# Optimization experiments

Measured on AMD Instinct MI355X. Metric: run time of the kernel, lower is better.

Reference implementation:

```python
import jax, jax.numpy as jnp
import numpy as np

N = 100_000          # nodes
E = 1_600_000        # edges
ORIG = 92            # orig_atom_fea_len
NBR = 41             # nbr_fea_len (RBF bins)
ATOM = 64            # atom_fea_len
NCONV = 3
H = 128              # h_fea_len
OUT = 1
NGRAPH = 256         # graphs in batch
ZDIM = 2 * ATOM + NBR  # CGConv concat dim = 169
RBF_VMIN, RBF_VMAX = 0.0, 8.0


def setup_inputs() -> dict:
    key = jax.random.key(0)
    ks = jax.random.split(key, 12)
    s = lambda fan: float(1.0 / np.sqrt(fan))
    u = lambda k, shape, fan: jax.random.uniform(k, shape, jnp.float32, -s(fan), s(fan))
    return {
        "x": jax.random.normal(ks[0], (N, ORIG), jnp.float32),
        "edge_attr": jax.random.normal(ks[1], (E, 3), jnp.float32),
        "W_emb": u(ks[2], (ORIG, ATOM), ORIG),
        "b_emb": u(ks[3], (ATOM,), ORIG),
        "Wf": u(ks[4], (NCONV, ZDIM, ATOM), ZDIM),
        "bf": u(ks[5], (NCONV, ATOM), ZDIM),
        "Ws": u(ks[6], (NCONV, ZDIM, ATOM), ZDIM),
        "bs": u(ks[7], (NCONV, ATOM), ZDIM),
        "bn_gamma": jnp.ones((NCONV, ATOM), jnp.float32),
        "bn_beta": jnp.zeros((NCONV, ATOM), jnp.float32),
        "W1": u(ks[8], (ATOM, H), ATOM),
        "b1": u(ks[9], (H,), ATOM),
        "W2": u(ks[10], (H, OUT), H),
        "b2": u(ks[11], (OUT,), H),
        "edge_index": jax.random.randint(jax.random.fold_in(key, 100), (2, E), 0, N),
        "batch": jnp.sort(jax.random.randint(jax.random.fold_in(key, 101), (N,), 0, NGRAPH)),
    }


def reference(x, edge_attr, W_emb, b_emb, Wf, bf, Ws, bs, bn_gamma, bn_beta,
              W1, b1, W2, b2, edge_index, batch):
    # atom embedding
    h = x @ W_emb + b_emb                                  # [N, ATOM]
    # edge distance -> RBF expansion (vmin=0, vmax=8, bins=NBR)
    d = jnp.sqrt(jnp.sum(edge_attr * edge_attr, axis=-1))  # [E]
    centers = jnp.linspace(RBF_VMIN, RBF_VMAX, NBR)
    gamma_rbf = 1.0 / ((RBF_VMAX - RBF_VMIN) / (NBR - 1))  # 1/lengthscale
    e = jnp.exp(-gamma_rbf * (d[:, None] - centers) ** 2)  # [E, NBR]

    src, dst = edge_index[0], edge_index[1]  # flow source->target: x_j = h[src], x_i = h[dst]
    for l in range(NCONV):
        # CGConv message: z = [x_i || x_j || e]; gate * core, scatter-add to i
        z = jnp.concatenate([h[dst], h[src], e], axis=-1)       # [E, ZDIM]
        msg = jax.nn.sigmoid(z @ Wf[l] + bf[l]) * jax.nn.softplus(z @ Ws[l] + bs[l])
        agg = jax.ops.segment_sum(msg, dst, num_segments=N)     # [N, ATOM]
        # BatchNorm (training-mode batch stats, eps=1e-5) then residual
        mu = agg.mean(axis=0)
        var = agg.var(axis=0)
        agg = bn_gamma[l] * (agg - mu) / jnp.sqrt(var + 1e-5) + bn_beta[l]
        h = jax.nn.softplus(agg + h)
    # global_add_pool over graphs, then MLP head
    g = jax.ops.segment_sum(h, batch, num_segments=NGRAPH)      # [NGRAPH, ATOM]
    out = jax.nn.softplus(g @ W1 + b1) @ W2 + b2                # [NGRAPH, OUT]
    return out
```

## Files before the change

kernel.cpp:

```cpp
#include <hip/hip_runtime.h>
#include <hip/hip_bf16.h>
#include <math.h>

#define N_NODES 100000
#define N_EDGES 1600000
#define ORIG    92
#define NBR     41
#define ATOM    64
#define NCONV   3
#define HFEA    128
#define NGRAPH  256
#define ZD      169
#define TBINS   5120
#define TMAX    10.0f
#define TS      ((TBINS + 1) * 64)
#define SP      72
#define SPE     136
#define NPBLK   128
#define LOG2E   1.4426950408889634f
#define LN2     0.6931471805599453f
#define NBKT    391
#define S1E     6250
#define S3CH    4096

typedef __attribute__((ext_vector_type(8))) short short8;
typedef __attribute__((ext_vector_type(4))) float f32x4;
typedef __attribute__((ext_vector_type(8))) int int8v;

__device__ __forceinline__ float softplus_f(float x) {
    return fmaxf(x, 0.0f) + log1pf(expf(-fabsf(x)));
}
__device__ __forceinline__ float sp_fast2(float x) {
    float t = x * LOG2E;
    return LN2 * (fmaxf(t, 0.0f) +
                  __builtin_amdgcn_logf(1.0f + __builtin_amdgcn_exp2f(-fabsf(t))));
}
__device__ __forceinline__ unsigned int pk_bf16(float lo, float hi) {
    unsigned int r;
    asm("v_cvt_pk_bf16_f32 %0, %1, %2" : "=v"(r) : "v"(lo), "v"(hi));
    return r;
}
__device__ __forceinline__ float bf_lo(unsigned int p) { return __uint_as_float(p << 16); }
__device__ __forceinline__ float bf_hi(unsigned int p) { return __uint_as_float(p & 0xffff0000u); }

__global__ __launch_bounds__(256) void k_bhist(const int* __restrict__ ei,
                                               int* __restrict__ bucketCnt,
                                               int* __restrict__ flag,
                                               int* __restrict__ bucketBase,
                                               int* __restrict__ bucketCursor,
                                               int* __restrict__ offs) {
    __shared__ int cntL[NBKT];
    __shared__ int lastFlag;
    int tid = threadIdx.x;
    for (int i = tid; i < NBKT; i += 256) cntL[i] = 0;
    __syncthreads();
    int base = blockIdx.x * S1E;
    for (int i = tid; i < S1E; i += 256)
        atomicAdd(&cntL[ei[N_EDGES + base + i] >> 8], 1);
    __syncthreads();
    for (int i = tid; i < NBKT; i += 256)
        if (cntL[i]) atomicAdd(&bucketCnt[i], cntL[i]);
    if (tid == 0) {
        __threadfence();
        lastFlag = (atomicAdd(flag, 1) == 255) ? 1 : 0;
    }
    __syncthreads();
    if (lastFlag && tid < 64) {
        __threadfence();
        int carry = 0;
        for (int b0 = 0; b0 < NBKT; b0 += 64) {
            int idx = b0 + tid;
            int v0 = (idx < NBKT) ? bucketCnt[idx] : 0;
            int v = v0;
            for (int d = 1; d < 64; d <<= 1) {
                int u = __shfl_up(v, d, 64);
                if (tid >= d) v += u;
            }
            if (idx < NBKT) {
                int ex = carry + v - v0;
                bucketBase[idx] = ex;
                bucketCursor[idx] = ex;
            }
            carry += __shfl(v, 63, 64);
        }
        if (tid == 0) {
            bucketBase[NBKT] = N_EDGES;
            offs[N_NODES] = N_EDGES;
        }
    }
}

__global__ __launch_bounds__(256) void k_psort1(const int* __restrict__ ei,
                                                const float* __restrict__ ea,
                                                int* __restrict__ bucketCursor,
                                                int2* __restrict__ staging) {
    __shared__ int cntL[NBKT], scanB[NBKT], curL[NBKT], gbaseL[NBKT];
    __shared__ int sortedD[S3CH], sortedN[S3CH];
    int tid = threadIdx.x;
    int base = blockIdx.x * S3CH;
    int myCount = N_EDGES - base;
    if (myCount > S3CH) myCount = S3CH;
    for (int i = tid; i < NBKT; i += 256) { cntL[i] = 0; curL[i] = 0; }
    __syncthreads();
    int descr[16], dstr[16];
#pragma unroll
    for (int j = 0; j < 16; ++j) {
        int i = j * 256 + tid;
        descr[j] = 0; dstr[j] = -1;
        if (i < myCount) {
            int e = base + i;
            int src = ei[e];
            int dst = ei[N_EDGES + e];
            float a = ea[3 * e], bb = ea[3 * e + 1], c = ea[3 * e + 2];
            float d = sqrtf(a * a + bb * bb + c * c);
            int bin = (int)fminf(fmaf(d, (float)TBINS / TMAX, 0.5f), (float)TBINS);
            descr[j] = (bin << 17) | src;
            dstr[j] = dst;
            atomicAdd(&cntL[dst >> 8], 1);
        }
    }
    __syncthreads();
    if (tid < 64) {
        int carry = 0;
        for (int b0 = 0; b0 < NBKT; b0 += 64) {
            int idx = b0 + tid;
            int v0 = (idx < NBKT) ? cntL[idx] : 0;
            int v = v0;
            for (int d = 1; d < 64; d <<= 1) {
                int u = __shfl_up(v, d, 64);
                if (tid >= d) v += u;
            }
            if (idx < NBKT) scanB[idx] = carry + v - v0;
            carry += __shfl(v, 63, 64);
        }
    }
    __syncthreads();
#pragma unroll
    for (int j = 0; j < 16; ++j) {
        if (dstr[j] >= 0) {
            int b = dstr[j] >> 8;
            int pos = scanB[b] + atomicAdd(&curL[b], 1);
            sortedD[pos] = descr[j];
            sortedN[pos] = dstr[j];
        }
    }
    for (int i = tid; i < NBKT; i += 256)
        if (cntL[i] > 0) gbaseL[i] = atomicAdd(&bucketCursor[i], cntL[i]);
    __syncthreads();
    for (int i = tid; i < myCount; i += 256) {
        int n = sortedN[i];
        int b = n >> 8;
        int2 pr; pr.x = sortedD[i]; pr.y = n;
        staging[gbaseL[b] + (i - scanB[b])] = pr;
    }
}

__global__ __launch_bounds__(256) void k_psort2(const int* __restrict__ bucketBase,
                                                const int2* __restrict__ staging,
                                                int* __restrict__ edesc,
                                                int* __restrict__ offs) {
    __shared__ int cnt[256], sbase[256], cur[256];
    int b = blockIdx.x, tid = threadIdx.x;
    int base = bucketBase[b];
    int nb = bucketBase[b + 1] - base;
    cnt[tid] = 0; cur[tid] = 0;
    __syncthreads();
    for (int i = tid; i < nb; i += 256)
        atomicAdd(&cnt[staging[base + i].y & 255], 1);
    __syncthreads();
    int v = cnt[tid];
    sbase[tid] = v;
    __syncthreads();
    for (int d = 1; d < 256; d <<= 1) {
        int u = (tid >= d) ? sbase[tid - d] : 0;
        __syncthreads();
        sbase[tid] += u;
        __syncthreads();
    }
    int ex = sbase[tid] - v;
    int dst = (b << 8) + tid;
    if (dst < N_NODES) offs[dst] = base + ex;
    sbase[tid] = ex;
    __syncthreads();
    for (int i = tid; i < nb; i += 256) {
        int2 pr = staging[base + i];
        int local = pr.y & 255;
        int pos = base + sbase[local] + atomicAdd(&cur[local], 1);
        edesc[pos] = pr.x;
    }
}

__global__ __launch_bounds__(256) void k_table2(const float* __restrict__ Wf,
                                                const float* __restrict__ bf,
                                                const float* __restrict__ Ws,
                                                const float* __restrict__ bs,
                                                const float* __restrict__ We,
                                                unsigned int* __restrict__ Tp,
                                                unsigned int* __restrict__ Bp,
                                                unsigned int* __restrict__ BpE) {
    int tid = threadIdx.x;
    int l = blockIdx.y;
    if (blockIdx.x == 161) {
        int m = tid >> 6, c = tid & 63;
        const float* Wb = ((m & 2) ? Ws : Wf) + (size_t)l * ZD * ATOM + (m & 1) * ATOM * ATOM + c;
        unsigned int* dst = Bp + (size_t)l * 8192 + (size_t)tid * 32;
        for (int kp = 0; kp < 32; ++kp) {
            float w0 = Wb[(2 * kp) * ATOM] * LOG2E;
            float w1 = Wb[(2 * kp + 1) * ATOM] * LOG2E;
            dst[kp] = pk_bf16(w0, w1);
        }
        return;
    }
    if (blockIdx.x == 162) {
        if (l != 0) return;
        int n = tid & 63, q = tid >> 6;
        for (int kp = q * 16; kp < q * 16 + 16; ++kp) {
            int k0 = 2 * kp, k1 = 2 * kp + 1;
            float w0 = (k0 < ORIG) ? We[k0 * ATOM + n] : 0.f;
            float w1 = (k1 < ORIG) ? We[k1 * ATOM + n] : 0.f;
            BpE[(size_t)n * 64 + kp] = pk_bf16(w0, w1);
        }
        return;
    }
    __shared__ float Wc[NBR * 64], Wsc[NBR * 64], R[32 * NBR];
    int b0 = blockIdx.x * 32;
    const float* srcf = Wf + (size_t)l * ZD * ATOM + 2 * ATOM * ATOM;
    const float* srcs = Ws + (size_t)l * ZD * ATOM + 2 * ATOM * ATOM;
    for (int i = tid; i < NBR * 64; i += 256) {
        Wc[i] = srcf[i] * LOG2E;
        Wsc[i] = srcs[i] * LOG2E;
    }
    for (int i = tid; i < 32 * NBR; i += 256) {
        int bin = i / NBR, k = i - bin * NBR;
        float d = (b0 + bin) * (TMAX / TBINS);
        float diff = d - 0.2f * k;
        R[i] = expf(-5.0f * diff * diff);
    }
    __syncthreads();
    int c = tid & 63;
    float afb = bf[l * ATOM + c] * LOG2E, asb = bs[l * ATOM + c] * LOG2E;
#pragma unroll
    for (int it = 0; it < 8; ++it) {
        int bin = (tid >> 6) + 4 * it;
        int gb = b0 + bin;
        if (gb <= TBINS) {
            float af = afb, as = asb;
            for (int k = 0; k < NBR; ++k) {
                float r = R[bin * NBR + k];
                af += r * Wc[k * 64 + c];
                as += r * Wsc[k * 64 + c];
            }
            Tp[(size_t)l * TS + (size_t)gb * 64 + c] = pk_bf16(af, as);
        }
    }
}

__global__ __launch_bounds__(256) void k_embed_nodeP(const float* __restrict__ x,
                                                     const unsigned int* __restrict__ BpE,
                                                     const float* __restrict__ be,
                                                     const unsigned int* __restrict__ Bp,
                                                     float* __restrict__ h,
                                                     unsigned int* __restrict__ Pi,
                                                     unsigned int* __restrict__ Pj) {
    __shared__ char smem[46080];
    short* Ae = (short*)smem;
    short* Be = (short*)(smem + 17408);
    short* Bn = (short*)smem;
    short* An = (short*)(smem + 36864);
    int tid = threadIdx.x;
    int n0 = blockIdx.x * 64;
    for (int i = tid; i < 64 * 64; i += 256) {
        int r = i >> 6, kp = i & 63;
        int node = n0 + r;
        float2 v = make_float2(0.f, 0.f);
        if (node < N_NODES && kp < 46) v = ((const float2*)x)[(size_t)node * 46 + kp];
        *(unsigned int*)&Ae[r * SPE + kp * 2] = pk_bf16(v.x, v.y);
    }
    {
        const uint4* src = (const uint4*)BpE;
        for (int i = tid; i < 64 * 16; i += 256) {
            int row = i >> 4, q = i & 15;
            *(uint4*)&Be[row * SPE + q * 8] = src[i];
        }
    }
    __syncthreads();
    int lane = tid & 63, w = tid >> 6;
    int c15 = lane & 15, kb = lane >> 4;
    {
        short8 af[4];
#pragma unroll
        for (int s = 0; s < 4; ++s)
            af[s] = *(const short8*)&Ae[(16 * w + c15) * SPE + s * 32 + kb * 8];
        f32x4 acc[4];
#pragma unroll
        for (int t = 0; t < 4; ++t) acc[t] = (f32x4){0.f, 0.f, 0.f, 0.f};
#pragma unroll
        for (int t = 0; t < 4; ++t) {
#pragma unroll
            for (int s = 0; s < 4; ++s) {
                short8 bf8 = *(const short8*)&Be[(16 * t + c15) * SPE + s * 32 + kb * 8];
                acc[t] = __builtin_amdgcn_mfma_f32_16x16x32_bf16(af[s], bf8, acc[t], 0, 0, 0);
            }
        }
#pragma unroll
        for (int t = 0; t < 4; ++t) {
            float bias = be[16 * t + c15];
#pragma unroll
            for (int reg = 0; reg < 4; ++reg) {
                int row = 16 * w + kb * 4 + reg;
                int node = n0 + row;
                float v = acc[t][reg] + bias;
                if (node < N_NODES) h[(size_t)node * 64 + 16 * t + c15] = v;
                An[row * SP + 16 * t + c15] = (short)pk_bf16(v, v);
            }
        }
    }
    __syncthreads();
    {
        const uint4* src = (const uint4*)Bp;
        for (int i = tid; i < 2048; i += 256) {
            int row = i >> 3, j = i & 7;
            *(uint4*)&Bn[row * SP + j * 8] = src[row * 8 + j];
        }
    }
    __syncthreads();
    short8 af2[2];
#pragma unroll
    for (int s = 0; s < 2; ++s)
        af2[s] = *(const short8*)&An[(16 * w + c15) * SP + s * 32 + kb * 8];
    f32x4 acc2[16];
#pragma unroll
    for (int t = 0; t < 16; ++t) acc2[t] = (f32x4){0.f, 0.f, 0.f, 0.f};
#pragma unroll
    for (int t = 0; t < 16; ++t) {
#pragma unroll
        for (int s = 0; s < 2; ++s) {
            short8 bf8 = *(const short8*)&Bn[(16 * t + c15) * SP + s * 32 + kb * 8];
            acc2[t] = __builtin_amdgcn_mfma_f32_16x16x32_bf16(af2[s], bf8, acc2[t], 0, 0, 0);
        }
    }
#pragma unroll
    for (int t = 0; t < 4; ++t) {
#pragma unroll
        for (int reg = 0; reg < 4; ++reg) {
            int row = kb * 4 + reg;
            int node = n0 + 16 * w + row;
            if (node < N_NODES) {
                Pi[(size_t)node * 64 + 16 * t + c15] = pk_bf16(acc2[t][reg], acc2[t + 8][reg]);
                Pj[(size_t)node * 64 + 16 * t + c15] = pk_bf16(acc2[t + 4][reg], acc2[t + 12][reg]);
            }
        }
    }
}

__global__ __launch_bounds__(256) void k_nodeP_mfma(float* __restrict__ h,
                                                    const float* __restrict__ agg,
                                                    const float* __restrict__ ss,
                                                    const unsigned int* __restrict__ Bp,
                                                    int l,
                                                    unsigned int* __restrict__ Pi,
                                                    unsigned int* __restrict__ Pj) {
    __shared__ short A[64 * SP];
    __shared__ short B[256 * SP];
    int tid = threadIdx.x;
    int n0 = blockIdx.x * 64;
    for (int i = tid; i < 64 * 32; i += 256) {
        int r = i >> 5, kp = i & 31;
        int node = n0 + r;
        int gi = node * 32 + kp;
        float2 hv = make_float2(0.f, 0.f);
        if (node < N_NODES) {
            hv = ((const float2*)h)[gi];
            float2 av = ((const float2*)agg)[gi];
            int c = kp * 2;
            float x0 = ss[c] * av.x + ss[64 + c] + hv.x;
            float x1 = ss[c + 1] * av.y + ss[64 + c + 1] + hv.y;
            hv.x = sp_fast2(x0);
            hv.y = sp_fast2(x1);
            ((float2*)h)[gi] = hv;
        }
        *(unsigned int*)&A[r * SP + kp * 2] = pk_bf16(hv.x, hv.y);
    }
    {
        const uint4* src = (const uint4*)(Bp + (size_t)l * 8192);
        for (int i = tid; i < 2048; i += 256) {
            int row = i >> 3, j = i & 7;
            *(uint4*)&B[row * SP + j * 8] = src[row * 8 + j];
        }
    }
    __syncthreads();
    int lane = tid & 63, w = tid >> 6;
    int c15 = lane & 15, kb = lane >> 4;
    short8 af[2];
#pragma unroll
    for (int s = 0; s < 2; ++s)
        af[s] = *(const short8*)&A[(16 * w + c15) * SP + s * 32 + kb * 8];
    f32x4 acc[16];
#pragma unroll
    for (int t = 0; t < 16; ++t) acc[t] = (f32x4){0.f, 0.f, 0.f, 0.f};
#pragma unroll
    for (int t = 0; t < 16; ++t) {
#pragma unroll
        for (int s = 0; s < 2; ++s) {
            short8 bf8 = *(const short8*)&B[(16 * t + c15) * SP + s * 32 + kb * 8];
            acc[t] = __builtin_amdgcn_mfma_f32_16x16x32_bf16(af[s], bf8, acc[t], 0, 0, 0);
        }
    }
#pragma unroll
    for (int t = 0; t < 4; ++t) {
#pragma unroll
        for (int reg = 0; reg < 4; ++reg) {
            int row = kb * 4 + reg;
            int node = n0 + 16 * w + row;
            if (node < N_NODES) {
                Pi[(size_t)node * 64 + 16 * t + c15] = pk_bf16(acc[t][reg], acc[t + 8][reg]);
                Pj[(size_t)node * 64 + 16 * t + c15] = pk_bf16(acc[t + 4][reg], acc[t + 12][reg]);
            }
        }
    }
}

__global__ __launch_bounds__(256, 4) void k_edge_sorted(const int* __restrict__ offs,
                                                        const int* __restrict__ edesc,
                                                        const unsigned int* __restrict__ Pi,
                                                        const unsigned int* __restrict__ Pj,
                                                        const unsigned int* __restrict__ Tp,
                                                        float* __restrict__ agg) {
    int wid = (blockIdx.x * 256 + threadIdx.x) >> 6;
    int lane = threadIdx.x & 63;
    if (wid >= N_NODES) return;
    int uwid = __builtin_amdgcn_readfirstlane(wid);
    int2 kk;
    asm volatile("s_load_dwordx2 %0, %1, 0x0\n\ts_waitcnt lgkmcnt(0)"
                 : "=s"(kk) : "s"(offs + uwid));
    int ko = kk.x, ke = kk.y;
    unsigned int pi = Pi[(size_t)uwid * 64 + lane];
    float gi = bf_lo(pi), ci = bf_hi(pi);
    float acc = 0.0f;
    int lane4 = lane * 4;
    const char* PjB = (const char*)Pj;
    const char* TpB = (const char*)Tp;
    int k0 = ko;
    for (; k0 + 16 <= ke; k0 += 16) {
        int8v e0, e1;
        asm volatile(
            "s_load_dwordx8 %0, %2, 0x0\n\t"
            "s_load_dwordx8 %1, %2, 0x20\n\t"
            "s_waitcnt lgkmcnt(0)"
            : "=&s"(e0), "=&s"(e1)
            : "s"(edesc + k0));
        unsigned int pjv[16], tjv[16];
#pragma unroll
        for (int j = 0; j < 16; ++j) {
            int v = (j < 8) ? e0[j & 7] : e1[j & 7];
            int sb = (v & 0x1FFFF) << 8;
            int tb = (v >> 17) << 8;
            pjv[j] = *(const unsigned int*)(PjB + sb + lane4);
            tjv[j] = *(const unsigned int*)(TpB + tb + lane4);
        }
#pragma unroll
        for (int j = 0; j < 16; ++j) {
            float g = gi + bf_lo(pjv[j]) + bf_lo(tjv[j]);
            float c = ci + bf_hi(pjv[j]) + bf_hi(tjv[j]);
            float sg = __builtin_amdgcn_rcpf(1.0f + __builtin_amdgcn_exp2f(-g));
            float sp = fmaxf(c, 0.0f) + __builtin_amdgcn_logf(1.0f + __builtin_amdgcn_exp2f(-fabsf(c)));
            acc = fmaf(sg, sp, acc);
        }
    }
    if (k0 < ke) {
        int8v e0, e1;
        asm volatile(
            "s_load_dwordx8 %0, %2, 0x0\n\t"
            "s_load_dwordx8 %1, %2, 0x20\n\t"
            "s_waitcnt lgkmcnt(0)"
            : "=&s"(e0), "=&s"(e1)
            : "s"(edesc + k0));
        unsigned int pjv[16], tjv[16];
#pragma unroll
        for (int j = 0; j < 16; ++j) {
            if (k0 + j < ke) {
                int v = (j < 8) ? e0[j & 7] : e1[j & 7];
                int sb = (v & 0x1FFFF) << 8;
                int tb = (v >> 17) << 8;
                pjv[j] = *(const unsigned int*)(PjB + sb + lane4);
                tjv[j] = *(const unsigned int*)(TpB + tb + lane4);
            }
        }
#pragma unroll
        for (int j = 0; j < 16; ++j) {
            if (k0 + j < ke) {
                float g = gi + bf_lo(pjv[j]) + bf_lo(tjv[j]);
                float c = ci + bf_hi(pjv[j]) + bf_hi(tjv[j]);
                float sg = __builtin_amdgcn_rcpf(1.0f + __builtin_amdgcn_exp2f(-g));
                float sp = fmaxf(c, 0.0f) + __builtin_amdgcn_logf(1.0f + __builtin_amdgcn_exp2f(-fabsf(c)));
                acc = fmaf(sg, sp, acc);
            }
        }
    }
    agg[(size_t)uwid * 64 + lane] = acc * LN2;
}

__global__ __launch_bounds__(256) void k_bnstats2(const float* __restrict__ agg,
                                                  float* __restrict__ partial,
                                                  int* __restrict__ lcnt,
                                                  const float* __restrict__ gamma,
                                                  const float* __restrict__ beta,
                                                  int l, float* __restrict__ ss) {
    __shared__ f32x4 ls4[256], ls24[256];
    __shared__ float ls[128];
    __shared__ int lastFlag;
    int tid = threadIdx.x;
    const f32x4* agg4 = (const f32x4*)agg;
    f32x4 s = (f32x4){0.f, 0.f, 0.f, 0.f};
    f32x4 s2 = (f32x4){0.f, 0.f, 0.f, 0.f};
    for (int i = blockIdx.x * 256 + tid; i < N_NODES * 16; i += NPBLK * 256) {
        f32x4 v = agg4[i];
        s += v;
        s2 += v * v;
    }
    ls4[tid] = s; ls24[tid] = s2;
    __syncthreads();
    for (int d = 128; d >= 16; d >>= 1) {
        if (tid < d) { ls4[tid] += ls4[tid + d]; ls24[tid] += ls24[tid + d]; }
        __syncthreads();
    }
    if (tid < 16) {
#pragma unroll
        for (int j = 0; j < 4; ++j) {
            partial[blockIdx.x * 128 + tid * 4 + j] = ls4[tid][j];
            partial[blockIdx.x * 128 + 64 + tid * 4 + j] = ls24[tid][j];
        }
    }
    __syncthreads();
    if (tid == 0) {
        __threadfence();
        lastFlag = (atomicAdd(lcnt, 1) == NPBLK - 1) ? 1 : 0;
    }
    __syncthreads();
    if (lastFlag) {
        __threadfence();
        if (tid < 128) {
            float sum = 0.0f;
            for (int b = 0; b < NPBLK; ++b) sum += partial[b * 128 + tid];
            ls[tid] = sum;
        }
        __syncthreads();
        if (tid < 64) {
            const float inv = 1.0f / (float)N_NODES;
            float mu = ls[tid] * inv;
            float var = ls[64 + tid] * inv - mu * mu;
            float sc = gamma[l * ATOM + tid] * rsqrtf(var + 1e-5f);
            ss[tid] = sc;
            ss[64 + tid] = beta[l * ATOM + tid] - mu * sc;
        }
    }
}

__global__ __launch_bounds__(256) void k_pool2(const float* __restrict__ agg,
                                               const float* __restrict__ ss,
                                               const float* __restrict__ h,
                                               const int* __restrict__ batch,
                                               float* __restrict__ g) {
    int w = threadIdx.x >> 6, lane = threadIdx.x & 63;
    int nbase = blockIdx.x * 64 + w * 16;
    float acc = 0.0f;
    int curg = -1;
    float sc = ss[lane], sh = ss[64 + lane];
    for (int i = 0; i < 16; ++i) {
        int n = nbase + i;
        if (n >= N_NODES) break;
        int gid = __builtin_amdgcn_readfirstlane(batch[n]);
        if (gid != curg) {
            if (curg >= 0) atomicAdd(&g[(size_t)curg * ATOM + lane], acc);
            curg = gid;
            acc = 0.0f;
        }
        float x = sc * agg[(size_t)n * 64 + lane] + sh + h[(size_t)n * 64 + lane];
        acc += sp_fast2(x);
    }
    if (curg >= 0) atomicAdd(&g[(size_t)curg * ATOM + lane], acc);
}

__global__ __launch_bounds__(128) void k_head(const float* __restrict__ g,
                                              const float* __restrict__ W1,
                                              const float* __restrict__ b1,
                                              const float* __restrict__ W2,
                                              const float* __restrict__ b2,
                                              float* __restrict__ out) {
    __shared__ float red[128];
    int gid = blockIdx.x, j = threadIdx.x;
    float acc = b1[j];
    for (int k = 0; k < ATOM; ++k) acc += g[gid * ATOM + k] * W1[k * HFEA + j];
    red[j] = softplus_f(acc) * W2[j];
    __syncthreads();
    for (int s = 64; s > 0; s >>= 1) {
        if (j < s) red[j] += red[j + s];
        __syncthreads();
    }
    if (j == 0) out[gid] = red[0] + b2[0];
}

extern "C" void kernel_launch(void* const* d_in, const int* in_sizes, int n_in,
                              void* d_out, int out_size, void* d_ws, size_t ws_size,
                              hipStream_t stream) {
    const float* x       = (const float*)d_in[0];
    const float* ea      = (const float*)d_in[1];
    const float* W_emb   = (const float*)d_in[2];
    const float* b_emb   = (const float*)d_in[3];
    const float* Wf      = (const float*)d_in[4];
    const float* bf      = (const float*)d_in[5];
    const float* Ws      = (const float*)d_in[6];
    const float* bs      = (const float*)d_in[7];
    const float* bn_g    = (const float*)d_in[8];
    const float* bn_b    = (const float*)d_in[9];
    const float* W1      = (const float*)d_in[10];
    const float* b1      = (const float*)d_in[11];
    const float* W2      = (const float*)d_in[12];
    const float* b2      = (const float*)d_in[13];
    const int*   ei      = (const int*)d_in[14];
    const int*   batch   = (const int*)d_in[15];
    float* out = (float*)d_out;

    char* wsb = (char*)d_ws;
    size_t off = 0;
    auto alloc = [&](size_t bytes) { char* p = wsb + off; off += (bytes + 255) & ~(size_t)255; return p; };
    float*        h        = (float*)alloc((size_t)N_NODES * 64 * 4);
    float*        agg      = (float*)alloc((size_t)N_NODES * 64 * 4);
    unsigned int* Pi       = (unsigned int*)alloc((size_t)N_NODES * 64 * 4);
    unsigned int* Pj       = (unsigned int*)alloc((size_t)N_NODES * 64 * 4);
    int*          edesc    = (int*)alloc((size_t)(N_EDGES + 16) * 4);
    int2*         staging  = (int2*)alloc((size_t)N_EDGES * 8);
    int*          meta     = (int*)alloc(1024 * 4);
    int*          bucketCnt    = meta;
    int*          lcnt         = meta + 512;
    int*          bucketBase   = (int*)alloc(520 * 4);
    int*          bucketCursor = (int*)alloc(512 * 4);
    int*          offs     = (int*)alloc((size_t)(N_NODES + 1) * 4);
    unsigned int* Tp       = (unsigned int*)alloc((size_t)NCONV * TS * 4);
    unsigned int* Bp       = (unsigned int*)alloc((size_t)NCONV * 8192 * 4);
    unsigned int* BpE      = (unsigned int*)alloc((size_t)64 * 64 * 4);
    float*        partial  = (float*)alloc((size_t)NPBLK * 128 * 4);
    float*        ss       = (float*)alloc(128 * 4);
    float*        g        = (float*)alloc((size_t)NGRAPH * 64 * 4);

    (void)hipMemsetAsync(meta, 0, 1024 * 4, stream);
    k_bhist<<<256, 256, 0, stream>>>(ei, bucketCnt, lcnt + 3, bucketBase, bucketCursor, offs);
    k_psort1<<<(N_EDGES + S3CH - 1) / S3CH, 256, 0, stream>>>(ei, ea, bucketCursor, staging);
    k_psort2<<<NBKT, 256, 0, stream>>>(bucketBase, staging, edesc, offs);

    dim3 tg(163, NCONV);
    k_table2<<<tg, 256, 0, stream>>>(Wf, bf, Ws, bs, W_emb, Tp, Bp, BpE);
    k_embed_nodeP<<<(N_NODES + 63) / 64, 256, 0, stream>>>(x, BpE, b_emb, Bp, h, Pi, Pj);

    for (int l = 0; l < NCONV; ++l) {
        if (l > 0)
            k_nodeP_mfma<<<(N_NODES + 63) / 64, 256, 0, stream>>>(h, agg, ss, Bp, l, Pi, Pj);
        k_edge_sorted<<<(N_NODES * 64 + 255) / 256, 256, 0, stream>>>(
            offs, edesc, Pi, Pj, Tp + (size_t)l * TS, agg);
        k_bnstats2<<<NPBLK, 256, 0, stream>>>(agg, partial, lcnt + l, bn_g, bn_b, l, ss);
    }

    (void)hipMemsetAsync(g, 0, (size_t)NGRAPH * 64 * 4, stream);
    k_pool2<<<(N_NODES + 63) / 64, 256, 0, stream>>>(agg, ss, h, batch, g);
    k_head<<<NGRAPH, 128, 0, stream>>>(g, W1, b1, W2, b2, out);
}
```

Baseline: 445.4 us.

## Fuse BatchNorm statistics into edge aggregation kernel via slotted atomics

The edge aggregation kernel now reduces per-block sums and sums of squares in shared memory and atomically adds them into 128 striped slots. This replaces the separate stats kernel that re-read the whole agg buffer. A tiny single-block kernel sums the slots, zeroes them for the next layer and computes the scale and shift. The LN2 factor is dropped from agg and folded into a rescaled epsilon, which BatchNorm's scale invariance allows. The node kernel also moves to float4 loads and stores. The cost is atomic contention and a block-wide sync in the edge kernel, and the grid now assumes N*64 divides by 256 exactly.

```diff
diff --git a/kernel.cpp b/kernel.cpp
--- a/kernel.cpp
+++ b/kernel.cpp
@@ -16,12 +16,13 @@
 #define TS      ((TBINS + 1) * 64)
 #define SP      72
 #define SPE     136
-#define NPBLK   128
 #define LOG2E   1.4426950408889634f
 #define LN2     0.6931471805599453f
+#define EPS2    (1e-5f / (LN2 * LN2))
 #define NBKT    391
 #define S1E     6250
 #define S3CH    4096
+#define PSLOT   128
 
 typedef __attribute__((ext_vector_type(8))) short short8;
 typedef __attribute__((ext_vector_type(4))) float f32x4;
@@ -364,22 +365,24 @@
     __shared__ short B[256 * SP];
     int tid = threadIdx.x;
     int n0 = blockIdx.x * 64;
-    for (int i = tid; i < 64 * 32; i += 256) {
-        int r = i >> 5, kp = i & 31;
+    for (int i = tid; i < 64 * 16; i += 256) {
+        int r = i >> 4, kq = i & 15;
         int node = n0 + r;
-        int gi = node * 32 + kp;
-        float2 hv = make_float2(0.f, 0.f);
+        float4 hv = make_float4(0.f, 0.f, 0.f, 0.f);
         if (node < N_NODES) {
-            hv = ((const float2*)h)[gi];
-            float2 av = ((const float2*)agg)[gi];
-            int c = kp * 2;
-            float x0 = ss[c] * av.x + ss[64 + c] + hv.x;
-            float x1 = ss[c + 1] * av.y + ss[64 + c + 1] + hv.y;
-            hv.x = sp_fast2(x0);
-            hv.y = sp_fast2(x1);
-            ((float2*)h)[gi] = hv;
-        }
-        *(unsigned int*)&A[r * SP + kp * 2] = pk_bf16(hv.x, hv.y);
+            hv = ((const float4*)h)[(size_t)node * 16 + kq];
+            float4 av = ((const float4*)agg)[(size_t)node * 16 + kq];
+            int c = kq * 4;
+            hv.x = sp_fast2(ss[c] * av.x + ss[64 + c] + hv.x);
+            hv.y = sp_fast2(ss[c + 1] * av.y + ss[64 + c + 1] + hv.y);
+            hv.z = sp_fast2(ss[c + 2] * av.z + ss[64 + c + 2] + hv.z);
+            hv.w = sp_fast2(ss[c + 3] * av.w + ss[64 + c + 3] + hv.w);
+            ((float4*)h)[(size_t)node * 16 + kq] = hv;
+        }
+        uint2 pk2;
+        pk2.x = pk_bf16(hv.x, hv.y);
+        pk2.y = pk_bf16(hv.z, hv.w);
+        *(uint2*)&A[r * SP + kq * 4] = pk2;
     }
     {
         const uint4* src = (const uint4*)(Bp + (size_t)l * 8192);
@@ -425,10 +428,12 @@
                                                         const unsigned int* __restrict__ Pi,
                                                         const unsigned int* __restrict__ Pj,
                                                         const unsigned int* __restrict__ Tp,
-                                                        float* __restrict__ agg) {
+                                                        float* __restrict__ agg,
+                                                        float* __restrict__ pstats) {
+    __shared__ float es[4][64], es2[4][64];
     int wid = (blockIdx.x * 256 + threadIdx.x) >> 6;
     int lane = threadIdx.x & 63;
-    if (wid >= N_NODES) return;
+    int w = threadIdx.x >> 6;
     int uwid = __builtin_amdgcn_readfirstlane(wid);
     int2 kk;
     asm volatile("s_load_dwordx2 %0, %1, 0x0\n\ts_waitcnt lgkmcnt(0)"
@@ -497,62 +502,37 @@
             }
         }
     }
-    agg[(size_t)uwid * 64 + lane] = acc * LN2;
-}
-
-__global__ __launch_bounds__(256) void k_bnstats2(const float* __restrict__ agg,
-                                                  float* __restrict__ partial,
-                                                  int* __restrict__ lcnt,
-                                                  const float* __restrict__ gamma,
-                                                  const float* __restrict__ beta,
-                                                  int l, float* __restrict__ ss) {
-    __shared__ f32x4 ls4[256], ls24[256];
+    agg[(size_t)uwid * 64 + lane] = acc;
+    es[w][lane] = acc;
+    es2[w][lane] = acc * acc;
+    __syncthreads();
+    if (threadIdx.x < 64) {
+        float s = es[0][threadIdx.x] + es[1][threadIdx.x] + es[2][threadIdx.x] + es[3][threadIdx.x];
+        float s2 = es2[0][threadIdx.x] + es2[1][threadIdx.x] + es2[2][threadIdx.x] + es2[3][threadIdx.x];
+        float* slot = pstats + (size_t)(blockIdx.x & (PSLOT - 1)) * 128;
+        atomicAdd(&slot[threadIdx.x], s);
+        atomicAdd(&slot[64 + threadIdx.x], s2);
+    }
+}
+
+__global__ __launch_bounds__(128) void k_bnfinal(float* __restrict__ pstats,
+                                                 const float* __restrict__ gamma,
+                                                 const float* __restrict__ beta,
+                                                 int l, float* __restrict__ ss) {
     __shared__ float ls[128];
-    __shared__ int lastFlag;
-    int tid = threadIdx.x;
-    const f32x4* agg4 = (const f32x4*)agg;
-    f32x4 s = (f32x4){0.f, 0.f, 0.f, 0.f};
-    f32x4 s2 = (f32x4){0.f, 0.f, 0.f, 0.f};
-    for (int i = blockIdx.x * 256 + tid; i < N_NODES * 16; i += NPBLK * 256) {
-        f32x4 v = agg4[i];
-        s += v;
-        s2 += v * v;
-    }
-    ls4[tid] = s; ls24[tid] = s2;
-    __syncthreads();
-    for (int d = 128; d >= 16; d >>= 1) {
-        if (tid < d) { ls4[tid] += ls4[tid + d]; ls24[tid] += ls24[tid + d]; }
-        __syncthreads();
-    }
-    if (tid < 16) {
-#pragma unroll
-        for (int j = 0; j < 4; ++j) {
-            partial[blockIdx.x * 128 + tid * 4 + j] = ls4[tid][j];
-            partial[blockIdx.x * 128 + 64 + tid * 4 + j] = ls24[tid][j];
-        }
-    }
-    __syncthreads();
-    if (tid == 0) {
-        __threadfence();
-        lastFlag = (atomicAdd(lcnt, 1) == NPBLK - 1) ? 1 : 0;
-    }
-    __syncthreads();
-    if (lastFlag) {
-        __threadfence();
-        if (tid < 128) {
-            float sum = 0.0f;
-            for (int b = 0; b < NPBLK; ++b) sum += partial[b * 128 + tid];
-            ls[tid] = sum;
-        }
-        __syncthreads();
-        if (tid < 64) {
-            const float inv = 1.0f / (float)N_NODES;
-            float mu = ls[tid] * inv;
-            float var = ls[64 + tid] * inv - mu * mu;
-            float sc = gamma[l * ATOM + tid] * rsqrtf(var + 1e-5f);
-            ss[tid] = sc;
-            ss[64 + tid] = beta[l * ATOM + tid] - mu * sc;
-        }
+    int t = threadIdx.x;
+    float sum = 0.0f;
+    for (int b = 0; b < PSLOT; ++b) sum += pstats[b * 128 + t];
+    ls[t] = sum;
+    for (int b = t; b < PSLOT * 128; b += 128) pstats[b] = 0.0f;
+    __syncthreads();
+    if (t < 64) {
+        const float inv = 1.0f / (float)N_NODES;
+        float mu = ls[t] * inv;
+        float var = ls[64 + t] * inv - mu * mu;
+        float sc = gamma[l * ATOM + t] * rsqrtf(var + EPS2);
+        ss[t] = sc;
+        ss[64 + t] = beta[l * ATOM + t] - mu * sc;
     }
 }
 
@@ -630,21 +610,21 @@
     unsigned int* Pj       = (unsigned int*)alloc((size_t)N_NODES * 64 * 4);
     int*          edesc    = (int*)alloc((size_t)(N_EDGES + 16) * 4);
     int2*         staging  = (int2*)alloc((size_t)N_EDGES * 8);
-    int*          meta     = (int*)alloc(1024 * 4);
+    int*          meta     = (int*)alloc((1024 + PSLOT * 128) * 4);
     int*          bucketCnt    = meta;
-    int*          lcnt         = meta + 512;
+    int*          flag         = meta + 512;
+    float*        pstats       = (float*)(meta + 1024);
     int*          bucketBase   = (int*)alloc(520 * 4);
     int*          bucketCursor = (int*)alloc(512 * 4);
     int*          offs     = (int*)alloc((size_t)(N_NODES + 1) * 4);
     unsigned int* Tp       = (unsigned int*)alloc((size_t)NCONV * TS * 4);
     unsigned int* Bp       = (unsigned int*)alloc((size_t)NCONV * 8192 * 4);
     unsigned int* BpE      = (unsigned int*)alloc((size_t)64 * 64 * 4);
-    float*        partial  = (float*)alloc((size_t)NPBLK * 128 * 4);
     float*        ss       = (float*)alloc(128 * 4);
     float*        g        = (float*)alloc((size_t)NGRAPH * 64 * 4);
 
-    (void)hipMemsetAsync(meta, 0, 1024 * 4, stream);
-    k_bhist<<<256, 256, 0, stream>>>(ei, bucketCnt, lcnt + 3, bucketBase, bucketCursor, offs);
+    (void)hipMemsetAsync(meta, 0, (1024 + PSLOT * 128) * 4, stream);
+    k_bhist<<<256, 256, 0, stream>>>(ei, bucketCnt, flag, bucketBase, bucketCursor, offs);
     k_psort1<<<(N_EDGES + S3CH - 1) / S3CH, 256, 0, stream>>>(ei, ea, bucketCursor, staging);
     k_psort2<<<NBKT, 256, 0, stream>>>(bucketBase, staging, edesc, offs);
 
@@ -655,9 +635,9 @@
     for (int l = 0; l < NCONV; ++l) {
         if (l > 0)
             k_nodeP_mfma<<<(N_NODES + 63) / 64, 256, 0, stream>>>(h, agg, ss, Bp, l, Pi, Pj);
-        k_edge_sorted<<<(N_NODES * 64 + 255) / 256, 256, 0, stream>>>(
-            offs, edesc, Pi, Pj, Tp + (size_t)l * TS, agg);
-        k_bnstats2<<<NPBLK, 256, 0, stream>>>(agg, partial, lcnt + l, bn_g, bn_b, l, ss);
+        k_edge_sorted<<<N_NODES * 64 / 256, 256, 0, stream>>>(
+            offs, edesc, Pi, Pj, Tp + (size_t)l * TS, agg, pstats);
+        k_bnfinal<<<1, 128, 0, stream>>>(pstats, bn_g, bn_b, l, ss);
     }
 
     (void)hipMemsetAsync(g, 0, (size_t)NGRAPH * 64 * 4, stream);
```

Result: faster. 404.5 us (-9.2%).
